# Optimization experiments

Measured on AMD Instinct MI355X. Metric: run time of the kernel, lower is better.

Reference implementation:

```python
import jax, jax.numpy as jnp
import numpy as np


def setup_inputs() -> dict:
    key = jax.random.key(0)
    k1, k2, k3, k4 = jax.random.split(key, 4)
    n_entity, n_rel, dim = 2048, 32, 512
    entities = jax.random.normal(k1, (n_entity, dim), dtype=jnp.float32)
    relations = jax.random.normal(k2, (n_rel, dim), dtype=jnp.float32)
    W = jax.random.normal(k3, (dim, dim), dtype=jnp.float32) * (1.0 / np.sqrt(dim))
    b = jax.random.normal(k4, (dim,), dtype=jnp.float32) * 0.01
    return {"entities": entities, "relations": relations, "W": W, "b": b}


def reference(entities, relations, W, b):
    # gate_nn applied to both entities and relations (shared Linear)
    E = entities @ W.T + b            # [n_entity, dim]
    R = relations @ W.T + b           # [n_rel, dim]
    # Diagonal RESCAL: scores[e, r, f] = sum_d E[e,d] * R[r,d] * E[f,d]
    # Equivalent to the per-relation loop E @ diag(R_r) @ E^T, fused into one einsum.
    scores = jnp.einsum('ed,rd,fd->erf', E, R, E)  # [n_entity, n_rel, n_entity]
    return scores
```

## Files before the change

### kernel.cpp

```cpp
#include <hip/hip_runtime.h>

typedef __attribute__((ext_vector_type(8))) __bf16 bf16x8;
typedef __attribute__((ext_vector_type(4))) float f32x4;

__device__ __forceinline__ float bf2f(unsigned int u) {
    return __uint_as_float(u << 16);
}
__device__ __forceinline__ unsigned short f2bf(float f) {
    unsigned int x = __float_as_uint(f);
    return (unsigned short)((x + 0x7fffu + ((x >> 16) & 1u)) >> 16);
}

__global__ void cast_all(const float* __restrict__ ent, const float* __restrict__ rel,
                         const float* __restrict__ W,
                         unsigned short* __restrict__ X_bf,
                         unsigned short* __restrict__ W_bf) {
    int i = blockIdx.x * blockDim.x + threadIdx.x;
    const float* src;
    unsigned short* dst;
    int g;
    if (i < 262144) {
        src = ent; dst = X_bf; g = i;
    } else if (i < 266240) {
        src = rel; dst = X_bf + 2048 * 512; g = i - 262144;
    } else {
        if (i >= 331776) return;
        src = W; dst = W_bf; g = i - 266240;
    }
    float4 v = reinterpret_cast<const float4*>(src)[g];
    ushort4 o;
    o.x = f2bf(v.x); o.y = f2bf(v.y); o.z = f2bf(v.z); o.w = f2bf(v.w);
    reinterpret_cast<ushort4*>(dst)[g] = o;
}

__device__ __forceinline__ unsigned int mul2bf(unsigned int a, unsigned int b) {
    float a0 = bf2f(a & 0xffffu), a1 = bf2f(a >> 16);
    float b0 = bf2f(b & 0xffffu), b1 = bf2f(b >> 16);
    return (unsigned int)f2bf(a0 * b0) | ((unsigned int)f2bf(a1 * b1) << 16);
}

__global__ void build_ap(const unsigned short* __restrict__ G,
                         unsigned short* __restrict__ Ap) {
    int t = blockIdx.x * blockDim.x + threadIdx.x;
    int row = t >> 6;
    int d = (t & 63) * 8;
    int e = row >> 5, r = row & 31;
    const uint4 ev = *reinterpret_cast<const uint4*>(G + e * 512 + d);
    const uint4 rv = *reinterpret_cast<const uint4*>(G + (2048 + r) * 512 + d);
    uint4 o;
    o.x = mul2bf(ev.x, rv.x);
    o.y = mul2bf(ev.y, rv.y);
    o.z = mul2bf(ev.z, rv.z);
    o.w = mul2bf(ev.w, rv.w);
    *reinterpret_cast<uint4*>(Ap + (size_t)row * 512 + d) = o;
}

#define BM 128
#define BN 128
#define BK 64

template <bool GUARD_M, bool BIAS_BF16OUT>
__global__ __launch_bounds__(256, 2) void mfma_gemm_bt(
    const unsigned short* __restrict__ A,
    const unsigned short* __restrict__ Bt,
    const float* __restrict__ bias,
    void* __restrict__ Cout,
    int M, int N, int K) {
    __shared__ __align__(16) unsigned short As[BM * BK];
    __shared__ __align__(16) unsigned short Bs[BN * BK];

    const int tid = threadIdx.x;
    const int lane = tid & 63;
    const int wave = tid >> 6;
    const int nbn = N / BN;
    const int bm0 = (blockIdx.x / nbn) * BM;
    const int bn0 = (blockIdx.x % nbn) * BN;
    const int wr = wave >> 1, wc = wave & 1;

    f32x4 acc[4][4] = {};

    const int srow = wave * 32 + (lane >> 3);
    const int scol = (lane & 7) * 8;

    for (int kb = 0; kb < K; kb += BK) {
#pragma unroll
        for (int i = 0; i < 4; ++i) {
            int row = bm0 + srow + i * 8;
            if (GUARD_M) row = min(row, M - 1);
            const unsigned short* src = A + (size_t)row * K + kb + scol;
            unsigned short* dst = &As[(wave * 32 + i * 8) * BK];
            __builtin_amdgcn_global_load_lds(
                (const __attribute__((address_space(1))) void*)src,
                (__attribute__((address_space(3))) void*)dst, 16, 0, 0);
        }
#pragma unroll
        for (int i = 0; i < 4; ++i) {
            int row = bn0 + srow + i * 8;
            const unsigned short* src = Bt + (size_t)row * K + kb + scol;
            unsigned short* dst = &Bs[(wave * 32 + i * 8) * BK];
            __builtin_amdgcn_global_load_lds(
                (const __attribute__((address_space(1))) void*)src,
                (__attribute__((address_space(3))) void*)dst, 16, 0, 0);
        }
        __syncthreads();

#pragma unroll
        for (int ks = 0; ks < BK / 32; ++ks) {
            const int k0 = ks * 32 + (lane >> 4) * 8;
            bf16x8 av[4], bv[4];
#pragma unroll
            for (int m = 0; m < 4; ++m)
                av[m] = *reinterpret_cast<const bf16x8*>(
                    &As[(wr * 64 + m * 16 + (lane & 15)) * BK + k0]);
#pragma unroll
            for (int n = 0; n < 4; ++n)
                bv[n] = *reinterpret_cast<const bf16x8*>(
                    &Bs[(wc * 64 + n * 16 + (lane & 15)) * BK + k0]);
#pragma unroll
            for (int m = 0; m < 4; ++m)
#pragma unroll
                for (int n = 0; n < 4; ++n)
                    acc[m][n] = __builtin_amdgcn_mfma_f32_16x16x32_bf16(
                        av[m], bv[n], acc[m][n], 0, 0, 0);
        }
        __syncthreads();
    }

#pragma unroll
    for (int m = 0; m < 4; ++m) {
#pragma unroll
        for (int n = 0; n < 4; ++n) {
#pragma unroll
            for (int j = 0; j < 4; ++j) {
                int row = bm0 + wr * 64 + m * 16 + (lane >> 4) * 4 + j;
                int col = bn0 + wc * 64 + n * 16 + (lane & 15);
                if (GUARD_M && row >= M) continue;
                float v = acc[m][n][j];
                if (BIAS_BF16OUT) {
                    v += bias[col];
                    ((unsigned short*)Cout)[(size_t)row * N + col] = f2bf(v);
                } else {
                    ((float*)Cout)[(size_t)row * N + col] = v;
                }
            }
        }
    }
}

#define NT8 8

__global__ __launch_bounds__(512, 2) void gemm256_8ph(
    const unsigned short* __restrict__ A,
    const unsigned short* __restrict__ B,
    float* __restrict__ C) {
    __shared__ __align__(16) unsigned short lds[65536];

    const int tid = threadIdx.x;
    const int lane = tid & 63;
    const int wave = tid >> 6;
    const int wr = wave >> 2;
    const int wc = wave & 3;
    const int laneM = lane & 15;
    const int laneK = (lane >> 4) * 8;
    const int kx = (lane & 7) * 8;

    const int swz = (blockIdx.x & 7) * 256 + (blockIdx.x >> 3);
    const int bm0 = (swz >> 3) * 256;
    const int bn0 = (swz & 7) * 256;

    const int sr0 = tid >> 3;
    const int sc = ((tid & 7) * 8) ^ (((tid >> 3) & 7) * 8);

    auto STAGE = [&](const unsigned short* mat, int row0, int kb, int slotOff) {
#pragma unroll
        for (int rd = 0; rd < 2; ++rd) {
            const unsigned short* src = mat + (size_t)(row0 + sr0 + rd * 64) * 512 + kb + sc;
            unsigned short* dst = &lds[slotOff + wave * 512 + rd * 4096];
            __builtin_amdgcn_global_load_lds(
                (const __attribute__((address_space(1))) void*)src,
                (__attribute__((address_space(3))) void*)dst, 16, 0, 0);
        }
    };
    auto RD = [&](int slotOff, int r, int ks) -> bf16x8 {
        return *reinterpret_cast<const bf16x8*>(
            &lds[slotOff + r * 64 + (((ks * 32) + laneK) ^ kx)]);
    };

    f32x4 acc[8][4] = {};
    bf16x8 av[4][2], bv0[2][2], bv1[2][2];

    STAGE(A, bm0,        0, 0 * 32768 + 0 * 8192);
    STAGE(B, bn0,        0, 0 * 32768 + 16384 + 0 * 8192);
    STAGE(B, bn0 + 128,  0, 0 * 32768 + 16384 + 1 * 8192);
    STAGE(A, bm0 + 128,  0, 0 * 32768 + 1 * 8192);
    STAGE(B, bn0,       64, 1 * 32768 + 16384 + 0 * 8192);
    STAGE(A, bm0,       64, 1 * 32768 + 0 * 8192);
    STAGE(B, bn0 + 128, 64, 1 * 32768 + 16384 + 1 * 8192);
    asm volatile("s_waitcnt vmcnt(6)" ::: "memory");
    __builtin_amdgcn_s_barrier();

#pragma unroll
    for (int t = 0; t < NT8; ++t) {
        const int P = t & 1;
        const int sA = P * 32768 + wr * 8192;
        const int sB = P * 32768 + 16384 + (wc >> 1) * 8192;
        const int rB = (wc & 1) * 64;

#pragma unroll
        for (int m = 0; m < 4; ++m)
#pragma unroll
            for (int ks = 0; ks < 2; ++ks)
                av[m][ks] = RD(sA, m * 16 + laneM, ks);
#pragma unroll
        for (int n = 0; n < 2; ++n)
#pragma unroll
            for (int ks = 0; ks < 2; ++ks)
                bv0[n][ks] = RD(sB, rB + n * 16 + laneM, ks);
        if (t + 1 < NT8)
            STAGE(A, bm0 + 128, (t + 1) * 64, ((t + 1) & 1) * 32768 + 8192);
        __builtin_amdgcn_s_barrier();
        asm volatile("s_waitcnt lgkmcnt(0)" ::: "memory");
        __builtin_amdgcn_sched_barrier(0);
        __builtin_amdgcn_s_setprio(1);
#pragma unroll
        for (int ks = 0; ks < 2; ++ks)
#pragma unroll
            for (int m = 0; m < 4; ++m)
#pragma unroll
                for (int n = 0; n < 2; ++n)
                    acc[m][n] = __builtin_amdgcn_mfma_f32_16x16x32_bf16(
                        av[m][ks], bv0[n][ks], acc[m][n], 0, 0, 0);
        __builtin_amdgcn_s_setprio(0);
        __builtin_amdgcn_s_barrier();

#pragma unroll
        for (int n = 0; n < 2; ++n)
#pragma unroll
            for (int ks = 0; ks < 2; ++ks)
                bv1[n][ks] = RD(sB, rB + (2 + n) * 16 + laneM, ks);
        __builtin_amdgcn_s_barrier();
        asm volatile("s_waitcnt lgkmcnt(0)" ::: "memory");
        __builtin_amdgcn_sched_barrier(0);
        __builtin_amdgcn_s_setprio(1);
#pragma unroll
        for (int ks = 0; ks < 2; ++ks)
#pragma unroll
            for (int m = 0; m < 4; ++m)
#pragma unroll
                for (int n = 0; n < 2; ++n)
                    acc[m][2 + n] = __builtin_amdgcn_mfma_f32_16x16x32_bf16(
                        av[m][ks], bv1[n][ks], acc[m][2 + n], 0, 0, 0);
        __builtin_amdgcn_s_setprio(0);
        __builtin_amdgcn_s_barrier();

#pragma unroll
        for (int m = 0; m < 4; ++m)
#pragma unroll
            for (int ks = 0; ks < 2; ++ks)
                av[m][ks] = RD(sA, 64 + m * 16 + laneM, ks);
        if (t + 2 < NT8)
            STAGE(B, bn0, (t + 2) * 64, ((t + 2) & 1) * 32768 + 16384);
        __builtin_amdgcn_s_barrier();
        asm volatile("s_waitcnt lgkmcnt(0)" ::: "memory");
        __builtin_amdgcn_sched_barrier(0);
        __builtin_amdgcn_s_setprio(1);
#pragma unroll
        for (int ks = 0; ks < 2; ++ks)
#pragma unroll
            for (int m = 0; m < 4; ++m)
#pragma unroll
                for (int n = 0; n < 2; ++n)
                    acc[4 + m][2 + n] = __builtin_amdgcn_mfma_f32_16x16x32_bf16(
                        av[m][ks], bv1[n][ks], acc[4 + m][2 + n], 0, 0, 0);
        __builtin_amdgcn_s_setprio(0);
        __builtin_amdgcn_s_barrier();

        if (t + 2 < NT8) {
            STAGE(A, bm0, (t + 2) * 64, ((t + 2) & 1) * 32768);
            STAGE(B, bn0 + 128, (t + 2) * 64, ((t + 2) & 1) * 32768 + 16384 + 8192);
        }
        __builtin_amdgcn_s_barrier();
        __builtin_amdgcn_s_setprio(1);
#pragma unroll
        for (int ks = 0; ks < 2; ++ks)
#pragma unroll
            for (int m = 0; m < 4; ++m)
#pragma unroll
                for (int n = 0; n < 2; ++n)
                    acc[4 + m][n] = __builtin_amdgcn_mfma_f32_16x16x32_bf16(
                        av[m][ks], bv0[n][ks], acc[4 + m][n], 0, 0, 0);
        __builtin_amdgcn_s_setprio(0);
        if (t < NT8 - 1) {
            if (t == NT8 - 2)
                asm volatile("s_waitcnt vmcnt(0)" ::: "memory");
            else
                asm volatile("s_waitcnt vmcnt(6)" ::: "memory");
            __builtin_amdgcn_s_barrier();
        }
    }

#pragma unroll
    for (int mi = 0; mi < 8; ++mi)
#pragma unroll
        for (int ni = 0; ni < 4; ++ni)
#pragma unroll
            for (int j = 0; j < 4; ++j) {
                int row = bm0 + wr * 128 + mi * 16 + (lane >> 4) * 4 + j;
                int col = bn0 + wc * 64 + ni * 16 + laneM;
                __builtin_nontemporal_store(acc[mi][ni][j],
                                            &C[(size_t)row * 2048 + col]);
            }
}

extern "C" void kernel_launch(void* const* d_in, const int* in_sizes, int n_in,
                              void* d_out, int out_size, void* d_ws, size_t ws_size,
                              hipStream_t stream) {
    const float* entities  = (const float*)d_in[0];
    const float* relations = (const float*)d_in[1];
    const float* W         = (const float*)d_in[2];
    const float* b         = (const float*)d_in[3];

    char* ws = (char*)d_ws;
    unsigned short* W_bf = (unsigned short*)ws;
    unsigned short* X_bf = (unsigned short*)(ws + 524288);
    unsigned short* G_bf = (unsigned short*)(ws + 524288 + 2129920);
    unsigned short* Ap   = (unsigned short*)(ws + 524288 + 2129920 + 2129920);

    cast_all<<<1296, 256, 0, stream>>>(entities, relations, W, X_bf, W_bf);

    mfma_gemm_bt<true, true><<<17 * 4, 256, 0, stream>>>(
        X_bf, W_bf, b, (void*)G_bf, 2080, 512, 512);

    build_ap<<<16384, 256, 0, stream>>>(G_bf, Ap);

    gemm256_8ph<<<2048, 512, 0, stream>>>(Ap, G_bf, (float*)d_out);
}
```

Baseline: 238.2 us.

## Exploit score symmetry: compute lower-triangular tiles per relation and transpose-store mirror

Since scores[e,r,f] = scores[f,r,e], the main GEMM is restructured to run per relation over only the lower-triangular 256x256 tiles (36 per relation, 1152 blocks instead of 2048). Each off-diagonal tile writes its block directly, then transposes it through LDS with a swizzle and writes the mirrored block. The A operand layout is changed to relation-major so that each relation's 2048x512 slab is contiguous. This roughly halves the MFMA work, but the output write volume stays the same and the transposed stores add LDS traffic and extra synchronisation.

New measurement: 949.2 us. +298.5%, slower.

```diff
diff --git a/kernel.cpp b/kernel.cpp
--- a/kernel.cpp
+++ b/kernel.cpp
@@ -44,7 +44,7 @@
     int t = blockIdx.x * blockDim.x + threadIdx.x;
     int row = t >> 6;
     int d = (t & 63) * 8;
-    int e = row >> 5, r = row & 31;
+    int r = row >> 11, e = row & 2047;
     const uint4 ev = *reinterpret_cast<const uint4*>(G + e * 512 + d);
     const uint4 rv = *reinterpret_cast<const uint4*>(G + (2048 + r) * 512 + d);
     uint4 o;
@@ -149,9 +149,9 @@
 
 #define NT8 8
 
-__global__ __launch_bounds__(512, 2) void gemm256_8ph(
-    const unsigned short* __restrict__ A,
-    const unsigned short* __restrict__ B,
+__global__ __launch_bounds__(512, 2) void gemm256_tri(
+    const unsigned short* __restrict__ Ap,
+    const unsigned short* __restrict__ G,
     float* __restrict__ C) {
     __shared__ __align__(16) unsigned short lds[65536];
 
@@ -164,9 +164,16 @@
     const int laneK = (lane >> 4) * 8;
     const int kx = (lane & 7) * 8;
 
-    const int swz = (blockIdx.x & 7) * 256 + (blockIdx.x >> 3);
-    const int bm0 = (swz >> 3) * 256;
-    const int bn0 = (swz & 7) * 256;
+    const int swz = (blockIdx.x & 7) * 144 + (blockIdx.x >> 3);
+    const int r = swz / 36;
+    int t = swz - r * 36;
+    int ti = 0;
+    while (t >= ti + 1) { t -= ti + 1; ++ti; }
+    const int tj = t;
+    const int am0 = ti * 256;
+    const int bn0 = tj * 256;
+
+    const unsigned short* Ar = Ap + (size_t)r * 2048 * 512;
 
     const int sr0 = tid >> 3;
     const int sc = ((tid & 7) * 8) ^ (((tid >> 3) & 7) * 8);
@@ -181,27 +188,27 @@
                 (__attribute__((address_space(3))) void*)dst, 16, 0, 0);
         }
     };
-    auto RD = [&](int slotOff, int r, int ks) -> bf16x8 {
+    auto RD = [&](int slotOff, int rr, int ks) -> bf16x8 {
         return *reinterpret_cast<const bf16x8*>(
-            &lds[slotOff + r * 64 + (((ks * 32) + laneK) ^ kx)]);
+            &lds[slotOff + rr * 64 + (((ks * 32) + laneK) ^ kx)]);
     };
 
     f32x4 acc[8][4] = {};
     bf16x8 av[4][2], bv0[2][2], bv1[2][2];
 
-    STAGE(A, bm0,        0, 0 * 32768 + 0 * 8192);
-    STAGE(B, bn0,        0, 0 * 32768 + 16384 + 0 * 8192);
-    STAGE(B, bn0 + 128,  0, 0 * 32768 + 16384 + 1 * 8192);
-    STAGE(A, bm0 + 128,  0, 0 * 32768 + 1 * 8192);
-    STAGE(B, bn0,       64, 1 * 32768 + 16384 + 0 * 8192);
-    STAGE(A, bm0,       64, 1 * 32768 + 0 * 8192);
-    STAGE(B, bn0 + 128, 64, 1 * 32768 + 16384 + 1 * 8192);
+    STAGE(Ar, am0,        0, 0 * 32768 + 0 * 8192);
+    STAGE(G,  bn0,        0, 0 * 32768 + 16384 + 0 * 8192);
+    STAGE(G,  bn0 + 128,  0, 0 * 32768 + 16384 + 1 * 8192);
+    STAGE(Ar, am0 + 128,  0, 0 * 32768 + 1 * 8192);
+    STAGE(G,  bn0,       64, 1 * 32768 + 16384 + 0 * 8192);
+    STAGE(Ar, am0,       64, 1 * 32768 + 0 * 8192);
+    STAGE(G,  bn0 + 128, 64, 1 * 32768 + 16384 + 1 * 8192);
     asm volatile("s_waitcnt vmcnt(6)" ::: "memory");
     __builtin_amdgcn_s_barrier();
 
 #pragma unroll
-    for (int t = 0; t < NT8; ++t) {
-        const int P = t & 1;
+    for (int tt = 0; tt < NT8; ++tt) {
+        const int P = tt & 1;
         const int sA = P * 32768 + wr * 8192;
         const int sB = P * 32768 + 16384 + (wc >> 1) * 8192;
         const int rB = (wc & 1) * 64;
@@ -216,8 +223,8 @@
 #pragma unroll
             for (int ks = 0; ks < 2; ++ks)
                 bv0[n][ks] = RD(sB, rB + n * 16 + laneM, ks);
-        if (t + 1 < NT8)
-            STAGE(A, bm0 + 128, (t + 1) * 64, ((t + 1) & 1) * 32768 + 8192);
+        if (tt + 1 < NT8)
+            STAGE(Ar, am0 + 128, (tt + 1) * 64, ((tt + 1) & 1) * 32768 + 8192);
         __builtin_amdgcn_s_barrier();
         asm volatile("s_waitcnt lgkmcnt(0)" ::: "memory");
         __builtin_amdgcn_sched_barrier(0);
@@ -258,8 +265,8 @@
 #pragma unroll
             for (int ks = 0; ks < 2; ++ks)
                 av[m][ks] = RD(sA, 64 + m * 16 + laneM, ks);
-        if (t + 2 < NT8)
-            STAGE(B, bn0, (t + 2) * 64, ((t + 2) & 1) * 32768 + 16384);
+        if (tt + 2 < NT8)
+            STAGE(G, bn0, (tt + 2) * 64, ((tt + 2) & 1) * 32768 + 16384);
         __builtin_amdgcn_s_barrier();
         asm volatile("s_waitcnt lgkmcnt(0)" ::: "memory");
         __builtin_amdgcn_sched_barrier(0);
@@ -275,9 +282,9 @@
         __builtin_amdgcn_s_setprio(0);
         __builtin_amdgcn_s_barrier();
 
-        if (t + 2 < NT8) {
-            STAGE(A, bm0, (t + 2) * 64, ((t + 2) & 1) * 32768);
-            STAGE(B, bn0 + 128, (t + 2) * 64, ((t + 2) & 1) * 32768 + 16384 + 8192);
+        if (tt + 2 < NT8) {
+            STAGE(Ar, am0, (tt + 2) * 64, ((tt + 2) & 1) * 32768);
+            STAGE(G, bn0 + 128, (tt + 2) * 64, ((tt + 2) & 1) * 32768 + 16384 + 8192);
         }
         __builtin_amdgcn_s_barrier();
         __builtin_amdgcn_s_setprio(1);
@@ -290,8 +297,8 @@
                     acc[4 + m][n] = __builtin_amdgcn_mfma_f32_16x16x32_bf16(
                         av[m][ks], bv0[n][ks], acc[4 + m][n], 0, 0, 0);
         __builtin_amdgcn_s_setprio(0);
-        if (t < NT8 - 1) {
-            if (t == NT8 - 2)
+        if (tt < NT8 - 1) {
+            if (tt == NT8 - 2)
                 asm volatile("s_waitcnt vmcnt(0)" ::: "memory");
             else
                 asm volatile("s_waitcnt vmcnt(6)" ::: "memory");
@@ -299,17 +306,56 @@
         }
     }
 
+    const size_t rOff = (size_t)r * 2048;
+
 #pragma unroll
     for (int mi = 0; mi < 8; ++mi)
 #pragma unroll
         for (int ni = 0; ni < 4; ++ni)
 #pragma unroll
-            for (int j = 0; j < 4; ++j) {
-                int row = bm0 + wr * 128 + mi * 16 + (lane >> 4) * 4 + j;
-                int col = bn0 + wc * 64 + ni * 16 + laneM;
-                __builtin_nontemporal_store(acc[mi][ni][j],
-                                            &C[(size_t)row * 2048 + col]);
+            for (int jj = 0; jj < 4; ++jj) {
+                int e = ti * 256 + wr * 128 + mi * 16 + (lane >> 4) * 4 + jj;
+                int f = tj * 256 + wc * 64 + ni * 16 + laneM;
+                __builtin_nontemporal_store(acc[mi][ni][jj],
+                                            &C[(size_t)e * 65536 + rOff + f]);
             }
+
+    if (ti != tj) {
+        float* buf = (float*)lds;
+#pragma unroll
+        for (int h = 0; h < 2; ++h) {
+            __syncthreads();
+            if (wr == h) {
+#pragma unroll
+                for (int mi = 0; mi < 8; ++mi)
+#pragma unroll
+                    for (int ni = 0; ni < 4; ++ni)
+#pragma unroll
+                        for (int jj = 0; jj < 4; ++jj) {
+                            int lrow = mi * 16 + (lane >> 4) * 4 + jj;
+                            int lcol = wc * 64 + ni * 16 + laneM;
+                            buf[lrow * 256 + (lcol ^ ((lrow & 12) << 2))] =
+                                acc[mi][ni][jj];
+                        }
+            }
+            __syncthreads();
+            const int fl = tid >> 1;
+            const int eb = (tid & 1) * 64;
+#pragma unroll
+            for (int g = 0; g < 16; ++g) {
+                const int e0 = eb + g * 4;
+                const int sx = (e0 & 12) << 2;
+                f32x4 v;
+                v[0] = buf[(e0 + 0) * 256 + (fl ^ sx)];
+                v[1] = buf[(e0 + 1) * 256 + (fl ^ sx)];
+                v[2] = buf[(e0 + 2) * 256 + (fl ^ sx)];
+                v[3] = buf[(e0 + 3) * 256 + (fl ^ sx)];
+                __builtin_nontemporal_store(
+                    v, (f32x4*)&C[(size_t)(tj * 256 + fl) * 65536 + rOff +
+                                  ti * 256 + h * 128 + e0]);
+            }
+        }
+    }
 }
 
 extern "C" void kernel_launch(void* const* d_in, const int* in_sizes, int n_in,
@@ -333,5 +379,5 @@
 
     build_ap<<<16384, 256, 0, stream>>>(G_bf, Ap);
 
-    gemm256_8ph<<<2048, 512, 0, stream>>>(Ap, G_bf, (float*)d_out);
-}
+    gemm256_tri<<<1152, 512, 0, stream>>>(Ap, G_bf, (float*)d_out);
+}
```
